# Optimization experiments

Measured on AMD Instinct MI355X. Metric: run time of the kernel, lower is better.

Reference implementation:

```python
import jax, jax.numpy as jnp
import numpy as np

# RReLU in eval mode acts as leaky-relu with slope (lower+upper)/2, defaults 1/8, 1/3
RRELU_SLOPE = (1.0 / 8.0 + 1.0 / 3.0) / 2.0

T, N, F, H, C, O, E = 8, 50000, 128, 128, 64, 2, 800000
HM1 = H - 1  # second GCN layer / MLP input width = hidden_feat - 1


def _glorot(k, shape):
    a = np.sqrt(6.0 / (shape[-2] + shape[-1])).astype(np.float32)
    return jax.random.uniform(k, shape, jnp.float32, -a, a)


def setup_inputs() -> dict:
    key = jax.random.key(0)
    ks = jax.random.split(key, 16)
    inp = {}
    inp["feats"] = jax.random.normal(ks[0], (T, N, F), jnp.float32)
    inp["src"] = jax.random.randint(ks[1], (E,), 0, N, jnp.int32)
    inp["dst"] = jax.random.randint(ks[2], (E,), 0, N, jnp.int32)
    # initial GCN weights (xavier_uniform as in reset_parameters)
    inp["W1_0"] = _glorot(ks[3], (F, H))
    inp["W2_0"] = _glorot(ks[4], (H, HM1))
    # mat-GRU cell 1 (rows=F, cols=H): gates stacked [z, r, h]
    inp["g1_W"] = jax.random.normal(ks[5], (3, F, F), jnp.float32) * 0.05
    inp["g1_U"] = jax.random.normal(ks[6], (3, F, F), jnp.float32) * 0.05
    inp["g1_b"] = jnp.zeros((3, F, H), jnp.float32)
    # mat-GRU cell 2 (rows=H, cols=H-1)
    inp["g2_W"] = jax.random.normal(ks[7], (3, H, H), jnp.float32) * 0.05
    inp["g2_U"] = jax.random.normal(ks[8], (3, H, H), jnp.float32) * 0.05
    inp["g2_b"] = jnp.zeros((3, H, HM1), jnp.float32)
    # MLP head
    inp["mlp_w1"] = _glorot(ks[9], (HM1, C))
    inp["mlp_b1"] = jnp.zeros((C,), jnp.float32)
    inp["mlp_w2"] = _glorot(ks[10], (C, O))
    inp["mlp_b2"] = jnp.zeros((O,), jnp.float32)
    return inp


def _mat_gru(gW, gU, gb, Wh):
    # EvolveGCN-O: weight matrix is both input and hidden of the GRU
    z = jax.nn.sigmoid(gW[0] @ Wh + gU[0] @ Wh + gb[0])
    r = jax.nn.sigmoid(gW[1] @ Wh + gU[1] @ Wh + gb[1])
    h_til = jnp.tanh(gW[2] @ Wh + gU[2] @ (r * Wh) + gb[2])
    return (1.0 - z) * Wh + z * h_til


def reference(feats, W1_0, W2_0, g1_W, g1_U, g1_b, g2_W, g2_U, g2_b,
              mlp_w1, mlp_b1, mlp_w2, mlp_b2, src, dst):
    n = feats.shape[1]
    ones = jnp.ones(src.shape, jnp.float32)
    deg_out = jax.ops.segment_sum(ones, src, num_segments=n)
    deg_in = jax.ops.segment_sum(ones, dst, num_segments=n)
    # symmetric GCN normalization D_out^-1/2 A D_in^-1/2 on edge list
    norm = (jax.lax.rsqrt(jnp.maximum(deg_out, 1.0))[src]
            * jax.lax.rsqrt(jnp.maximum(deg_in, 1.0))[dst])  # [E]

    def aggregate(x):  # x: [N, d] -> [N, d]
        return jax.ops.segment_sum(x[src] * norm[:, None], dst, num_segments=n)

    def step(carry, x):
        W1, W2, _ = carry
        W1 = _mat_gru(g1_W, g1_U, g1_b, W1)
        W2 = _mat_gru(g2_W, g2_U, g2_b, W2)
        h1 = aggregate(x @ W1)                      # [N, H]
        h1 = jnp.where(h1 >= 0, h1, RRELU_SLOPE * h1)  # RReLU (eval-mode)
        h2 = aggregate(h1 @ W2)                     # [N, H-1]
        return (W1, W2, h2), None

    feat0 = jnp.zeros((n, W2_0.shape[1]), feats.dtype)
    (W1, W2, feat_end), _ = jax.lax.scan(step, (W1_0, W2_0, feat0), feats)
    out = jnp.maximum(feat_end @ mlp_w1 + mlp_b1, 0.0) @ mlp_w2 + mlp_b2
    return out
```

## Files before the change

### kernel.cpp

```cpp
#include <hip/hip_runtime.h>


#define HM1 127

static constexpr float RRELU_SLOPE = (1.0f / 8.0f + 1.0f / 3.0f) * 0.5f;

__device__ __forceinline__ float sigmoidf_(float x) {
    return 1.0f / (1.0f + expf(-x));
}

__global__ __launch_bounds__(256) void prep_gates(
    const float* __restrict__ g1W, const float* __restrict__ g1U,
    const float* __restrict__ g2W, const float* __restrict__ g2U,
    float* __restrict__ AT)
{
    int t = blockIdx.x * 256 + threadIdx.x;
    int m = t >> 14;
    int k = (t >> 7) & 127;
    int i = t & 127;
    const float* W = (m < 4) ? g1W : g2W;
    const float* U = (m < 4) ? g1U : g2U;
    int which = m & 3;
    float v;
    if (which == 0)      v = W[i * 128 + k] + U[i * 128 + k];
    else if (which == 1) v = W[16384 + i * 128 + k] + U[16384 + i * 128 + k];
    else if (which == 2) v = W[32768 + i * 128 + k];
    else                 v = U[32768 + i * 128 + k];
    AT[t] = v;
}

__global__ __launch_bounds__(128) void gru_evolve(
    const float* __restrict__ W1_0, const float* __restrict__ W2_0,
    const float* __restrict__ AT,
    const float* __restrict__ g1b, const float* __restrict__ g2b,
    float* __restrict__ W1f, float* __restrict__ W2f)
{
    const int i = threadIdx.x;
    const int bid = blockIdx.x;
    const int cell = (bid >= 128) ? 1 : 0;
    const int c = cell ? (bid - 128) : bid;

    const float* A  = AT + cell * 4 * 16384;
    const float* A0 = A;
    const float* A1 = A + 16384;
    const float* B0 = A + 32768;
    const float* B1 = A + 49152;
    const float* gb = cell ? g2b : g1b;
    const int   ldb = cell ? HM1 : 128;
    const float* W0 = cell ? W2_0 : W1_0;
    const int   ldw = cell ? HM1 : 128;

    __shared__ float w[128];
    __shared__ float rw[128];

    const float zb = gb[i * ldb + c];
    const float rb = gb[128 * ldb + i * ldb + c];
    const float hb = gb[2 * 128 * ldb + i * ldb + c];
    float wi = W0[i * ldw + c];
    w[i] = wi;
    __syncthreads();

    for (int s = 0; s < 8; ++s) {
        float zacc = zb, racc = rb, tacc = hb;
        #pragma unroll 4
        for (int k = 0; k < 128; ++k) {
            float wk = w[k];
            zacc += A0[k * 128 + i] * wk;
            racc += A1[k * 128 + i] * wk;
            tacc += B0[k * 128 + i] * wk;
        }
        float r = sigmoidf_(racc);
        rw[i] = r * wi;
        __syncthreads();
        #pragma unroll 4
        for (int k = 0; k < 128; ++k)
            tacc += B1[k * 128 + i] * rw[k];
        float z = sigmoidf_(zacc);
        float t = tanhf(tacc);
        float nwi = (1.0f - z) * wi + z * t;
        __syncthreads();
        wi = nwi;
        w[i] = nwi;
        __syncthreads();
    }

    float* Wf = cell ? W2f : W1f;
    Wf[i * 128 + c] = wi;
}

__global__ __launch_bounds__(256) void small_matmul(
    const float* __restrict__ W2f, const float* __restrict__ mw1,
    float* __restrict__ W2m)
{
    int idx = blockIdx.x * 256 + threadIdx.x;
    int i = idx >> 6, j = idx & 63;
    float acc = 0.0f;
    for (int k = 0; k < HM1; ++k)
        acc += W2f[i * 128 + k] * mw1[k * 64 + j];
    W2m[idx] = acc;
}

__global__ __launch_bounds__(256) void deg_count(
    const int* __restrict__ src, const int* __restrict__ dst,
    int* __restrict__ degO, int* __restrict__ degI, int E)
{
    int e = blockIdx.x * 256 + threadIdx.x;
    if (e < E) {
        atomicAdd(&degO[src[e]], 1);
        atomicAdd(&degI[dst[e]], 1);
    }
}

__global__ __launch_bounds__(256) void rdeg_kernel(
    const int* __restrict__ degO, const int* __restrict__ degI,
    float* __restrict__ rdegO, float* __restrict__ rdegI, int N)
{
    int n = blockIdx.x * 256 + threadIdx.x;
    if (n < N) {
        rdegO[n] = rsqrtf(fmaxf((float)degO[n], 1.0f));
        rdegI[n] = rsqrtf(fmaxf((float)degI[n], 1.0f));
    }
}

__global__ __launch_bounds__(1024) void scan_kernel(
    const int* __restrict__ degI, int* __restrict__ row_ptr, int N)
{
    __shared__ int sums[1024];
    const int t = threadIdx.x;
    const int chunk = (N + 1023) / 1024;
    const int lo = t * chunk;
    const int hi = min(lo + chunk, N);
    int s = 0;
    for (int i = lo; i < hi; ++i) s += degI[i];
    sums[t] = s;
    __syncthreads();
    for (int off = 1; off < 1024; off <<= 1) {
        int v = (t >= off) ? sums[t - off] : 0;
        __syncthreads();
        sums[t] += v;
        __syncthreads();
    }
    int base = (t > 0) ? sums[t - 1] : 0;
    for (int i = lo; i < hi; ++i) {
        row_ptr[i] = base;
        base += degI[i];
    }
    if (t == 1023) row_ptr[N] = sums[1023];
}

__global__ __launch_bounds__(256) void build_csr(
    const int* __restrict__ src, const int* __restrict__ dst,
    const int* __restrict__ row_ptr, int* __restrict__ cursor,
    int* __restrict__ srcs, int E)
{
    int e = blockIdx.x * 256 + threadIdx.x;
    if (e < E) {
        int d = dst[e];
        int pos = row_ptr[d] + atomicAdd(&cursor[d], 1);
        srcs[pos] = src[e];
    }
}

__global__ __launch_bounds__(256) void gather128(
    const float* __restrict__ x, const int* __restrict__ srcs,
    const int* __restrict__ row_ptr, const float* __restrict__ rdegO,
    const float* __restrict__ rdegI, float* __restrict__ out, int N)
{
    int n = (blockIdx.x * 256 + threadIdx.x) >> 6;
    int lane = threadIdx.x & 63;
    if (n >= N) return;
    int lo = row_ptr[n], hi = row_ptr[n + 1];
    float ax = 0.0f, ay = 0.0f;
    for (int base = lo; base < hi; base += 64) {
        int cnt = min(hi - base, 64);
        int idx   = (lane < cnt) ? srcs[base + lane] : 0;
        float wgt = (lane < cnt) ? rdegO[idx] : 0.0f;
        int j = 0;
        for (; j + 4 <= cnt; j += 4) {
            int s0 = __shfl(idx, j + 0), s1 = __shfl(idx, j + 1);
            int s2 = __shfl(idx, j + 2), s3 = __shfl(idx, j + 3);
            float w0 = __shfl(wgt, j + 0), w1 = __shfl(wgt, j + 1);
            float w2 = __shfl(wgt, j + 2), w3 = __shfl(wgt, j + 3);
            float2 v0 = *reinterpret_cast<const float2*>(x + (size_t)s0 * 128 + lane * 2);
            float2 v1 = *reinterpret_cast<const float2*>(x + (size_t)s1 * 128 + lane * 2);
            float2 v2 = *reinterpret_cast<const float2*>(x + (size_t)s2 * 128 + lane * 2);
            float2 v3 = *reinterpret_cast<const float2*>(x + (size_t)s3 * 128 + lane * 2);
            ax += w0 * v0.x + w1 * v1.x + w2 * v2.x + w3 * v3.x;
            ay += w0 * v0.y + w1 * v1.y + w2 * v2.y + w3 * v3.y;
        }
        for (; j < cnt; ++j) {
            int s0 = __shfl(idx, j);
            float w0 = __shfl(wgt, j);
            float2 v0 = *reinterpret_cast<const float2*>(x + (size_t)s0 * 128 + lane * 2);
            ax += w0 * v0.x;
            ay += w0 * v0.y;
        }
    }
    float ri = rdegI[n];
    float2 o; o.x = ax * ri; o.y = ay * ri;
    *reinterpret_cast<float2*>(out + (size_t)n * 128 + lane * 2) = o;
}

__global__ __launch_bounds__(256) void gemm_rrelu(
    const float* __restrict__ X, const float* __restrict__ W,
    float* __restrict__ Y, int N)
{
    int row = blockIdx.x * 256 + threadIdx.x;
    int c0 = blockIdx.y * 64;
    if (row >= N) return;

    float acc[64];
    #pragma unroll
    for (int j = 0; j < 64; ++j) acc[j] = 0.0f;

    const float4* xr = reinterpret_cast<const float4*>(X + (size_t)row * 128);
    for (int k4 = 0; k4 < 32; ++k4) {
        float4 xv = xr[k4];
        const float* wr = W + (k4 * 4) * 128 + c0;
        #pragma unroll
        for (int j = 0; j < 64; ++j) acc[j] += xv.x * wr[j];
        wr += 128;
        #pragma unroll
        for (int j = 0; j < 64; ++j) acc[j] += xv.y * wr[j];
        wr += 128;
        #pragma unroll
        for (int j = 0; j < 64; ++j) acc[j] += xv.z * wr[j];
        wr += 128;
        #pragma unroll
        for (int j = 0; j < 64; ++j) acc[j] += xv.w * wr[j];
    }

    float* yr = Y + (size_t)row * 128 + c0;
    #pragma unroll
    for (int j = 0; j < 64; j += 4) {
        float4 v;
        v.x = acc[j + 0] >= 0.0f ? acc[j + 0] : RRELU_SLOPE * acc[j + 0];
        v.y = acc[j + 1] >= 0.0f ? acc[j + 1] : RRELU_SLOPE * acc[j + 1];
        v.z = acc[j + 2] >= 0.0f ? acc[j + 2] : RRELU_SLOPE * acc[j + 2];
        v.w = acc[j + 3] >= 0.0f ? acc[j + 3] : RRELU_SLOPE * acc[j + 3];
        *reinterpret_cast<float4*>(yr + j) = v;
    }
}

__global__ __launch_bounds__(256) void gemm_y(
    const float* __restrict__ H1, const float* __restrict__ W2m,
    const float* __restrict__ rdegO, float* __restrict__ Ys, int N)
{
    int row = blockIdx.x * 256 + threadIdx.x;
    if (row >= N) return;

    float acc[64];
    #pragma unroll
    for (int j = 0; j < 64; ++j) acc[j] = 0.0f;

    const float4* hr = reinterpret_cast<const float4*>(H1 + (size_t)row * 128);
    for (int k4 = 0; k4 < 32; ++k4) {
        float4 h = hr[k4];
        const float* wr = W2m + (k4 * 4) * 64;
        #pragma unroll
        for (int j = 0; j < 64; ++j) acc[j] += h.x * wr[j];
        wr += 64;
        #pragma unroll
        for (int j = 0; j < 64; ++j) acc[j] += h.y * wr[j];
        wr += 64;
        #pragma unroll
        for (int j = 0; j < 64; ++j) acc[j] += h.z * wr[j];
        wr += 64;
        #pragma unroll
        for (int j = 0; j < 64; ++j) acc[j] += h.w * wr[j];
    }

    float ro = rdegO[row];
    float* yr = Ys + (size_t)row * 64;
    #pragma unroll
    for (int j = 0; j < 64; j += 4) {
        float4 v;
        v.x = acc[j] * ro; v.y = acc[j + 1] * ro;
        v.z = acc[j + 2] * ro; v.w = acc[j + 3] * ro;
        *reinterpret_cast<float4*>(yr + j) = v;
    }
}

__global__ __launch_bounds__(256) void gather64_mlp(
    const float* __restrict__ Ys, const int* __restrict__ srcs,
    const int* __restrict__ row_ptr, const float* __restrict__ rdegI,
    const float* __restrict__ b1, const float* __restrict__ w2,
    const float* __restrict__ b2, float* __restrict__ out, int N)
{
    int n = (blockIdx.x * 256 + threadIdx.x) >> 6;
    int lane = threadIdx.x & 63;
    if (n >= N) return;
    int lo = row_ptr[n], hi = row_ptr[n + 1];
    float acc = 0.0f;
    for (int base = lo; base < hi; base += 64) {
        int cnt = min(hi - base, 64);
        int idx = (lane < cnt) ? srcs[base + lane] : 0;
        int j = 0;
        for (; j + 4 <= cnt; j += 4) {
            int s0 = __shfl(idx, j + 0), s1 = __shfl(idx, j + 1);
            int s2 = __shfl(idx, j + 2), s3 = __shfl(idx, j + 3);
            acc += Ys[(size_t)s0 * 64 + lane] + Ys[(size_t)s1 * 64 + lane]
                 + Ys[(size_t)s2 * 64 + lane] + Ys[(size_t)s3 * 64 + lane];
        }
        for (; j < cnt; ++j) {
            int s0 = __shfl(idx, j);
            acc += Ys[(size_t)s0 * 64 + lane];
        }
    }
    float z = acc * rdegI[n];
    float t = fmaxf(z + b1[lane], 0.0f);
    float p0 = t * w2[lane * 2 + 0];
    float p1 = t * w2[lane * 2 + 1];
    #pragma unroll
    for (int off = 32; off; off >>= 1) {
        p0 += __shfl_xor(p0, off);
        p1 += __shfl_xor(p1, off);
    }
    if (lane == 0) {
        out[(size_t)n * 2 + 0] = p0 + b2[0];
        out[(size_t)n * 2 + 1] = p1 + b2[1];
    }
}

extern "C" void kernel_launch(void* const* d_in, const int* in_sizes, int n_in,
                              void* d_out, int out_size, void* d_ws, size_t ws_size,
                              hipStream_t stream) {
    const float* feats = (const float*)d_in[0];
    const int*   src   = (const int*)d_in[1];
    const int*   dst   = (const int*)d_in[2];
    const float* W1_0  = (const float*)d_in[3];
    const float* W2_0  = (const float*)d_in[4];
    const float* g1W   = (const float*)d_in[5];
    const float* g1U   = (const float*)d_in[6];
    const float* g1b   = (const float*)d_in[7];
    const float* g2W   = (const float*)d_in[8];
    const float* g2U   = (const float*)d_in[9];
    const float* g2b   = (const float*)d_in[10];
    const float* mw1   = (const float*)d_in[11];
    const float* mb1   = (const float*)d_in[12];
    const float* mw2   = (const float*)d_in[13];
    const float* mb2   = (const float*)d_in[14];
    float* out = (float*)d_out;

    const int E = in_sizes[1];
    const int N = in_sizes[0] / (8 * 128);

    float* ws    = (float*)d_ws;
    float* W1f   = ws;
    float* W2f   = W1f + 16384;
    float* W2m   = W2f + 16384;
    float* AT    = W2m + 8192;
    float* rdegO = AT + 8 * 16384;
    float* rdegI = rdegO + N;
    int*   degO  = (int*)(rdegI + N);
    int*   degI  = degO + N;
    int*   cursor= degI + N;
    int*   row_ptr = cursor + N;
    int*   srcs  = row_ptr + N + 1;
    float* Sx    = (float*)(srcs + E);
    float* H1    = Sx + (size_t)N * 128;
    float* Ys    = Sx;

    hipMemsetAsync(degO, 0, sizeof(int) * 3 * (size_t)N, stream);
    deg_count<<<(E + 255) / 256, 256, 0, stream>>>(src, dst, degO, degI, E);
    rdeg_kernel<<<(N + 255) / 256, 256, 0, stream>>>(degO, degI, rdegO, rdegI, N);
    scan_kernel<<<1, 1024, 0, stream>>>(degI, row_ptr, N);
    build_csr<<<(E + 255) / 256, 256, 0, stream>>>(src, dst, row_ptr, cursor, srcs, E);

    prep_gates<<<512, 256, 0, stream>>>(g1W, g1U, g2W, g2U, AT);
    gru_evolve<<<255, 128, 0, stream>>>(W1_0, W2_0, AT, g1b, g2b, W1f, W2f);
    small_matmul<<<32, 256, 0, stream>>>(W2f, mw1, W2m);

    const float* x7 = feats + (size_t)7 * N * 128;
    int ngather = ((N * 64) + 255) / 256;
    gather128<<<ngather, 256, 0, stream>>>(x7, srcs, row_ptr, rdegO, rdegI, Sx, N);

    dim3 gg((N + 255) / 256, 2);
    gemm_rrelu<<<gg, 256, 0, stream>>>(Sx, W1f, H1, N);
    gemm_y<<<(N + 255) / 256, 256, 0, stream>>>(H1, W2m, rdegO, Ys, N);

    gather64_mlp<<<ngather, 256, 0, stream>>>(Ys, srcs, row_ptr, rdegI,
                                              mb1, mw2, mb2, out, N);
}
```

Measured before the change: 726.6 us.

## Merge independent setup kernels into phases and apply first GEMM before gathering

Independent setup kernels (degree counting, gate prep, GRU evolution, scan, rdeg, CSR build, small matmul) are combined into three multi-role launches so independent work runs concurrently and fewer launches are issued. The first layer is reordered to compute X@W1 scaled by rdegO before aggregation, so the gather only sums and then applies rdegI and RReLU, which removes per-edge weight shuffles. The gather loops are unrolled by 8 for more loads in flight. The trade-offs are that the scan now runs in a single 256-thread block alongside the GRU blocks, and that the GEMM now runs in the same launch as the CSR build.

```diff
diff --git a/kernel.cpp b/kernel.cpp
--- a/kernel.cpp
+++ b/kernel.cpp
@@ -9,162 +9,200 @@
     return 1.0f / (1.0f + expf(-x));
 }
 
-__global__ __launch_bounds__(256) void prep_gates(
+__global__ __launch_bounds__(256) void phase1(
+    const int* __restrict__ src, const int* __restrict__ dst,
+    int* __restrict__ degO, int* __restrict__ degI, int E, int nbE,
     const float* __restrict__ g1W, const float* __restrict__ g1U,
     const float* __restrict__ g2W, const float* __restrict__ g2U,
     float* __restrict__ AT)
 {
-    int t = blockIdx.x * 256 + threadIdx.x;
-    int m = t >> 14;
-    int k = (t >> 7) & 127;
-    int i = t & 127;
-    const float* W = (m < 4) ? g1W : g2W;
-    const float* U = (m < 4) ? g1U : g2U;
-    int which = m & 3;
-    float v;
-    if (which == 0)      v = W[i * 128 + k] + U[i * 128 + k];
-    else if (which == 1) v = W[16384 + i * 128 + k] + U[16384 + i * 128 + k];
-    else if (which == 2) v = W[32768 + i * 128 + k];
-    else                 v = U[32768 + i * 128 + k];
-    AT[t] = v;
-}
-
-__global__ __launch_bounds__(128) void gru_evolve(
+    int bid = blockIdx.x;
+    if (bid < nbE) {
+        int e = bid * 256 + threadIdx.x;
+        if (e < E) {
+            atomicAdd(&degO[src[e]], 1);
+            atomicAdd(&degI[dst[e]], 1);
+        }
+    } else {
+        int t = (bid - nbE) * 256 + threadIdx.x;
+        int m = t >> 14;
+        int k = (t >> 7) & 127;
+        int i = t & 127;
+        const float* W = (m < 4) ? g1W : g2W;
+        const float* U = (m < 4) ? g1U : g2U;
+        int which = m & 3;
+        float v;
+        if (which == 0)      v = W[i * 128 + k] + U[i * 128 + k];
+        else if (which == 1) v = W[16384 + i * 128 + k] + U[16384 + i * 128 + k];
+        else if (which == 2) v = W[32768 + i * 128 + k];
+        else                 v = U[32768 + i * 128 + k];
+        AT[t] = v;
+    }
+}
+
+__global__ __launch_bounds__(256) void phase2(
     const float* __restrict__ W1_0, const float* __restrict__ W2_0,
     const float* __restrict__ AT,
     const float* __restrict__ g1b, const float* __restrict__ g2b,
-    float* __restrict__ W1f, float* __restrict__ W2f)
-{
-    const int i = threadIdx.x;
-    const int bid = blockIdx.x;
-    const int cell = (bid >= 128) ? 1 : 0;
-    const int c = cell ? (bid - 128) : bid;
-
-    const float* A  = AT + cell * 4 * 16384;
-    const float* A0 = A;
-    const float* A1 = A + 16384;
-    const float* B0 = A + 32768;
-    const float* B1 = A + 49152;
-    const float* gb = cell ? g2b : g1b;
-    const int   ldb = cell ? HM1 : 128;
-    const float* W0 = cell ? W2_0 : W1_0;
-    const int   ldw = cell ? HM1 : 128;
-
-    __shared__ float w[128];
-    __shared__ float rw[128];
-
-    const float zb = gb[i * ldb + c];
-    const float rb = gb[128 * ldb + i * ldb + c];
-    const float hb = gb[2 * 128 * ldb + i * ldb + c];
-    float wi = W0[i * ldw + c];
-    w[i] = wi;
-    __syncthreads();
-
-    for (int s = 0; s < 8; ++s) {
-        float zacc = zb, racc = rb, tacc = hb;
-        #pragma unroll 4
-        for (int k = 0; k < 128; ++k) {
-            float wk = w[k];
-            zacc += A0[k * 128 + i] * wk;
-            racc += A1[k * 128 + i] * wk;
-            tacc += B0[k * 128 + i] * wk;
-        }
-        float r = sigmoidf_(racc);
-        rw[i] = r * wi;
+    float* __restrict__ W1f, float* __restrict__ W2f,
+    const int* __restrict__ degO, const int* __restrict__ degI,
+    float* __restrict__ rdegO, float* __restrict__ rdegI,
+    int* __restrict__ row_ptr, int N)
+{
+    __shared__ float smem[512];
+    int bid = blockIdx.x;
+    if (bid < 128) {
+        const int half = threadIdx.x >> 7;
+        const int i = threadIdx.x & 127;
+        int c = bid * 2 + half;
+        if (c > 254) c = 254;
+        const int cell = (c >= 128) ? 1 : 0;
+        const int cc = cell ? (c - 128) : c;
+
+        const float* A  = AT + cell * 4 * 16384;
+        const float* A0 = A;
+        const float* A1 = A + 16384;
+        const float* B0 = A + 32768;
+        const float* B1 = A + 49152;
+        const float* gb = cell ? g2b : g1b;
+        const int   ldb = cell ? HM1 : 128;
+        const float* W0 = cell ? W2_0 : W1_0;
+        const int   ldw = cell ? HM1 : 128;
+
+        float* w  = smem + half * 128;
+        float* rw = smem + 256 + half * 128;
+
+        const float zb = gb[i * ldb + cc];
+        const float rb = gb[128 * ldb + i * ldb + cc];
+        const float hb = gb[2 * 128 * ldb + i * ldb + cc];
+        float wi = W0[i * ldw + cc];
+        w[i] = wi;
         __syncthreads();
-        #pragma unroll 4
-        for (int k = 0; k < 128; ++k)
-            tacc += B1[k * 128 + i] * rw[k];
-        float z = sigmoidf_(zacc);
-        float t = tanhf(tacc);
-        float nwi = (1.0f - z) * wi + z * t;
+
+        for (int s = 0; s < 8; ++s) {
+            float zacc = zb, racc = rb, tacc = hb;
+            #pragma unroll 4
+            for (int k = 0; k < 128; ++k) {
+                float wk = w[k];
+                zacc += A0[k * 128 + i] * wk;
+                racc += A1[k * 128 + i] * wk;
+                tacc += B0[k * 128 + i] * wk;
+            }
+            float r = sigmoidf_(racc);
+            rw[i] = r * wi;
+            __syncthreads();
+            #pragma unroll 4
+            for (int k = 0; k < 128; ++k)
+                tacc += B1[k * 128 + i] * rw[k];
+            float z = sigmoidf_(zacc);
+            float t = tanhf(tacc);
+            float nwi = (1.0f - z) * wi + z * t;
+            __syncthreads();
+            wi = nwi;
+            w[i] = nwi;
+            __syncthreads();
+        }
+        float* Wf = cell ? W2f : W1f;
+        Wf[i * 128 + cc] = wi;
+    } else if (bid == 128) {
+        int* sums = (int*)smem;
+        const int t = threadIdx.x;
+        const int chunk = (N + 255) / 256;
+        const int lo = t * chunk;
+        const int hi = min(lo + chunk, N);
+        int s = 0;
+        for (int i2 = lo; i2 < hi; ++i2) s += degI[i2];
+        sums[t] = s;
         __syncthreads();
-        wi = nwi;
-        w[i] = nwi;
-        __syncthreads();
-    }
-
-    float* Wf = cell ? W2f : W1f;
-    Wf[i * 128 + c] = wi;
-}
-
-__global__ __launch_bounds__(256) void small_matmul(
+        for (int off = 1; off < 256; off <<= 1) {
+            int v = (t >= off) ? sums[t - off] : 0;
+            __syncthreads();
+            sums[t] += v;
+            __syncthreads();
+        }
+        int base = (t > 0) ? sums[t - 1] : 0;
+        for (int i2 = lo; i2 < hi; ++i2) {
+            row_ptr[i2] = base;
+            base += degI[i2];
+        }
+        if (t == 255) row_ptr[N] = sums[255];
+    } else {
+        int n = (bid - 129) * 256 + threadIdx.x;
+        if (n < N) {
+            rdegO[n] = rsqrtf(fmaxf((float)degO[n], 1.0f));
+            rdegI[n] = rsqrtf(fmaxf((float)degI[n], 1.0f));
+        }
+    }
+}
+
+__global__ __launch_bounds__(256) void phase3(
+    const int* __restrict__ src, const int* __restrict__ dst,
+    const int* __restrict__ row_ptr, int* __restrict__ cursor,
+    int* __restrict__ srcs, int E, int nbE,
+    const float* __restrict__ x7, const float* __restrict__ W1f,
+    const float* __restrict__ rdegO, float* __restrict__ Zs, int N, int nbN,
     const float* __restrict__ W2f, const float* __restrict__ mw1,
     float* __restrict__ W2m)
 {
-    int idx = blockIdx.x * 256 + threadIdx.x;
-    int i = idx >> 6, j = idx & 63;
-    float acc = 0.0f;
-    for (int k = 0; k < HM1; ++k)
-        acc += W2f[i * 128 + k] * mw1[k * 64 + j];
-    W2m[idx] = acc;
-}
-
-__global__ __launch_bounds__(256) void deg_count(
-    const int* __restrict__ src, const int* __restrict__ dst,
-    int* __restrict__ degO, int* __restrict__ degI, int E)
-{
-    int e = blockIdx.x * 256 + threadIdx.x;
-    if (e < E) {
-        atomicAdd(&degO[src[e]], 1);
-        atomicAdd(&degI[dst[e]], 1);
-    }
-}
-
-__global__ __launch_bounds__(256) void rdeg_kernel(
-    const int* __restrict__ degO, const int* __restrict__ degI,
-    float* __restrict__ rdegO, float* __restrict__ rdegI, int N)
-{
-    int n = blockIdx.x * 256 + threadIdx.x;
-    if (n < N) {
-        rdegO[n] = rsqrtf(fmaxf((float)degO[n], 1.0f));
-        rdegI[n] = rsqrtf(fmaxf((float)degI[n], 1.0f));
-    }
-}
-
-__global__ __launch_bounds__(1024) void scan_kernel(
-    const int* __restrict__ degI, int* __restrict__ row_ptr, int N)
-{
-    __shared__ int sums[1024];
-    const int t = threadIdx.x;
-    const int chunk = (N + 1023) / 1024;
-    const int lo = t * chunk;
-    const int hi = min(lo + chunk, N);
-    int s = 0;
-    for (int i = lo; i < hi; ++i) s += degI[i];
-    sums[t] = s;
-    __syncthreads();
-    for (int off = 1; off < 1024; off <<= 1) {
-        int v = (t >= off) ? sums[t - off] : 0;
-        __syncthreads();
-        sums[t] += v;
-        __syncthreads();
-    }
-    int base = (t > 0) ? sums[t - 1] : 0;
-    for (int i = lo; i < hi; ++i) {
-        row_ptr[i] = base;
-        base += degI[i];
-    }
-    if (t == 1023) row_ptr[N] = sums[1023];
-}
-
-__global__ __launch_bounds__(256) void build_csr(
-    const int* __restrict__ src, const int* __restrict__ dst,
-    const int* __restrict__ row_ptr, int* __restrict__ cursor,
-    int* __restrict__ srcs, int E)
-{
-    int e = blockIdx.x * 256 + threadIdx.x;
-    if (e < E) {
-        int d = dst[e];
-        int pos = row_ptr[d] + atomicAdd(&cursor[d], 1);
-        srcs[pos] = src[e];
+    int bid = blockIdx.x;
+    if (bid < nbE) {
+        int e = bid * 256 + threadIdx.x;
+        if (e < E) {
+            int d = dst[e];
+            int pos = row_ptr[d] + atomicAdd(&cursor[d], 1);
+            srcs[pos] = src[e];
+        }
+    } else if (bid < nbE + 2 * nbN) {
+        int b = bid - nbE;
+        int half = b & 1;
+        int row = (b >> 1) * 256 + threadIdx.x;
+        int c0 = half * 64;
+        if (row >= N) return;
+
+        float acc[64];
+        #pragma unroll
+        for (int j = 0; j < 64; ++j) acc[j] = 0.0f;
+
+        const float4* xr = reinterpret_cast<const float4*>(x7 + (size_t)row * 128);
+        for (int k4 = 0; k4 < 32; ++k4) {
+            float4 xv = xr[k4];
+            const float* wr = W1f + (k4 * 4) * 128 + c0;
+            #pragma unroll
+            for (int j = 0; j < 64; ++j) acc[j] += xv.x * wr[j];
+            wr += 128;
+            #pragma unroll
+            for (int j = 0; j < 64; ++j) acc[j] += xv.y * wr[j];
+            wr += 128;
+            #pragma unroll
+            for (int j = 0; j < 64; ++j) acc[j] += xv.z * wr[j];
+            wr += 128;
+            #pragma unroll
+            for (int j = 0; j < 64; ++j) acc[j] += xv.w * wr[j];
+        }
+
+        float ro = rdegO[row];
+        float* zr = Zs + (size_t)row * 128 + c0;
+        #pragma unroll
+        for (int j = 0; j < 64; j += 4) {
+            float4 v;
+            v.x = acc[j] * ro; v.y = acc[j + 1] * ro;
+            v.z = acc[j + 2] * ro; v.w = acc[j + 3] * ro;
+            *reinterpret_cast<float4*>(zr + j) = v;
+        }
+    } else {
+        int idx = (bid - nbE - 2 * nbN) * 256 + threadIdx.x;
+        int i = idx >> 6, j = idx & 63;
+        float acc = 0.0f;
+        for (int k = 0; k < HM1; ++k)
+            acc += W2f[i * 128 + k] * mw1[k * 64 + j];
+        W2m[idx] = acc;
     }
 }
 
 __global__ __launch_bounds__(256) void gather128(
-    const float* __restrict__ x, const int* __restrict__ srcs,
-    const int* __restrict__ row_ptr, const float* __restrict__ rdegO,
-    const float* __restrict__ rdegI, float* __restrict__ out, int N)
+    const float* __restrict__ Zs, const int* __restrict__ srcs,
+    const int* __restrict__ row_ptr, const float* __restrict__ rdegI,
+    float* __restrict__ H1, int N)
 {
     int n = (blockIdx.x * 256 + threadIdx.x) >> 6;
     int lane = threadIdx.x & 63;
@@ -173,73 +211,37 @@
     float ax = 0.0f, ay = 0.0f;
     for (int base = lo; base < hi; base += 64) {
         int cnt = min(hi - base, 64);
-        int idx   = (lane < cnt) ? srcs[base + lane] : 0;
-        float wgt = (lane < cnt) ? rdegO[idx] : 0.0f;
+        int idx = (lane < cnt) ? srcs[base + lane] : 0;
         int j = 0;
-        for (; j + 4 <= cnt; j += 4) {
+        for (; j + 8 <= cnt; j += 8) {
             int s0 = __shfl(idx, j + 0), s1 = __shfl(idx, j + 1);
             int s2 = __shfl(idx, j + 2), s3 = __shfl(idx, j + 3);
-            float w0 = __shfl(wgt, j + 0), w1 = __shfl(wgt, j + 1);
-            float w2 = __shfl(wgt, j + 2), w3 = __shfl(wgt, j + 3);
-            float2 v0 = *reinterpret_cast<const float2*>(x + (size_t)s0 * 128 + lane * 2);
-            float2 v1 = *reinterpret_cast<const float2*>(x + (size_t)s1 * 128 + lane * 2);
-            float2 v2 = *reinterpret_cast<const float2*>(x + (size_t)s2 * 128 + lane * 2);
-            float2 v3 = *reinterpret_cast<const float2*>(x + (size_t)s3 * 128 + lane * 2);
-            ax += w0 * v0.x + w1 * v1.x + w2 * v2.x + w3 * v3.x;
-            ay += w0 * v0.y + w1 * v1.y + w2 * v2.y + w3 * v3.y;
+            int s4 = __shfl(idx, j + 4), s5 = __shfl(idx, j + 5);
+            int s6 = __shfl(idx, j + 6), s7 = __shfl(idx, j + 7);
+            float2 v0 = *reinterpret_cast<const float2*>(Zs + (size_t)s0 * 128 + lane * 2);
+            float2 v1 = *reinterpret_cast<const float2*>(Zs + (size_t)s1 * 128 + lane * 2);
+            float2 v2 = *reinterpret_cast<const float2*>(Zs + (size_t)s2 * 128 + lane * 2);
+            float2 v3 = *reinterpret_cast<const float2*>(Zs + (size_t)s3 * 128 + lane * 2);
+            float2 v4 = *reinterpret_cast<const float2*>(Zs + (size_t)s4 * 128 + lane * 2);
+            float2 v5 = *reinterpret_cast<const float2*>(Zs + (size_t)s5 * 128 + lane * 2);
+            float2 v6 = *reinterpret_cast<const float2*>(Zs + (size_t)s6 * 128 + lane * 2);
+            float2 v7 = *reinterpret_cast<const float2*>(Zs + (size_t)s7 * 128 + lane * 2);
+            ax += v0.x + v1.x + v2.x + v3.x + v4.x + v5.x + v6.x + v7.x;
+            ay += v0.y + v1.y + v2.y + v3.y + v4.y + v5.y + v6.y + v7.y;
         }
         for (; j < cnt; ++j) {
             int s0 = __shfl(idx, j);
-            float w0 = __shfl(wgt, j);
-            float2 v0 = *reinterpret_cast<const float2*>(x + (size_t)s0 * 128 + lane * 2);
-            ax += w0 * v0.x;
-            ay += w0 * v0.y;
+            float2 v0 = *reinterpret_cast<const float2*>(Zs + (size_t)s0 * 128 + lane * 2);
+            ax += v0.x;
+            ay += v0.y;
         }
     }
     float ri = rdegI[n];
-    float2 o; o.x = ax * ri; o.y = ay * ri;
-    *reinterpret_cast<float2*>(out + (size_t)n * 128 + lane * 2) = o;
-}
-
-__global__ __launch_bounds__(256) void gemm_rrelu(
-    const float* __restrict__ X, const float* __restrict__ W,
-    float* __restrict__ Y, int N)
-{
-    int row = blockIdx.x * 256 + threadIdx.x;
-    int c0 = blockIdx.y * 64;
-    if (row >= N) return;
-
-    float acc[64];
-    #pragma unroll
-    for (int j = 0; j < 64; ++j) acc[j] = 0.0f;
-
-    const float4* xr = reinterpret_cast<const float4*>(X + (size_t)row * 128);
-    for (int k4 = 0; k4 < 32; ++k4) {
-        float4 xv = xr[k4];
-        const float* wr = W + (k4 * 4) * 128 + c0;
-        #pragma unroll
-        for (int j = 0; j < 64; ++j) acc[j] += xv.x * wr[j];
-        wr += 128;
-        #pragma unroll
-        for (int j = 0; j < 64; ++j) acc[j] += xv.y * wr[j];
-        wr += 128;
-        #pragma unroll
-        for (int j = 0; j < 64; ++j) acc[j] += xv.z * wr[j];
-        wr += 128;
-        #pragma unroll
-        for (int j = 0; j < 64; ++j) acc[j] += xv.w * wr[j];
-    }
-
-    float* yr = Y + (size_t)row * 128 + c0;
-    #pragma unroll
-    for (int j = 0; j < 64; j += 4) {
-        float4 v;
-        v.x = acc[j + 0] >= 0.0f ? acc[j + 0] : RRELU_SLOPE * acc[j + 0];
-        v.y = acc[j + 1] >= 0.0f ? acc[j + 1] : RRELU_SLOPE * acc[j + 1];
-        v.z = acc[j + 2] >= 0.0f ? acc[j + 2] : RRELU_SLOPE * acc[j + 2];
-        v.w = acc[j + 3] >= 0.0f ? acc[j + 3] : RRELU_SLOPE * acc[j + 3];
-        *reinterpret_cast<float4*>(yr + j) = v;
-    }
+    ax *= ri; ay *= ri;
+    ax = ax >= 0.0f ? ax : RRELU_SLOPE * ax;
+    ay = ay >= 0.0f ? ay : RRELU_SLOPE * ay;
+    float2 o; o.x = ax; o.y = ay;
+    *reinterpret_cast<float2*>(H1 + (size_t)n * 128 + lane * 2) = o;
 }
 
 __global__ __launch_bounds__(256) void gemm_y(
@@ -296,11 +298,15 @@
         int cnt = min(hi - base, 64);
         int idx = (lane < cnt) ? srcs[base + lane] : 0;
         int j = 0;
-        for (; j + 4 <= cnt; j += 4) {
+        for (; j + 8 <= cnt; j += 8) {
             int s0 = __shfl(idx, j + 0), s1 = __shfl(idx, j + 1);
             int s2 = __shfl(idx, j + 2), s3 = __shfl(idx, j + 3);
+            int s4 = __shfl(idx, j + 4), s5 = __shfl(idx, j + 5);
+            int s6 = __shfl(idx, j + 6), s7 = __shfl(idx, j + 7);
             acc += Ys[(size_t)s0 * 64 + lane] + Ys[(size_t)s1 * 64 + lane]
-                 + Ys[(size_t)s2 * 64 + lane] + Ys[(size_t)s3 * 64 + lane];
+                 + Ys[(size_t)s2 * 64 + lane] + Ys[(size_t)s3 * 64 + lane]
+                 + Ys[(size_t)s4 * 64 + lane] + Ys[(size_t)s5 * 64 + lane]
+                 + Ys[(size_t)s6 * 64 + lane] + Ys[(size_t)s7 * 64 + lane];
         }
         for (; j < cnt; ++j) {
             int s0 = __shfl(idx, j);
@@ -344,6 +350,8 @@
 
     const int E = in_sizes[1];
     const int N = in_sizes[0] / (8 * 128);
+    const int nbE = (E + 255) / 256;
+    const int nbN = (N + 255) / 256;
 
     float* ws    = (float*)d_ws;
     float* W1f   = ws;
@@ -357,27 +365,28 @@
     int*   cursor= degI + N;
     int*   row_ptr = cursor + N;
     int*   srcs  = row_ptr + N + 1;
-    float* Sx    = (float*)(srcs + E);
-    float* H1    = Sx + (size_t)N * 128;
-    float* Ys    = Sx;
+    float* Zs    = (float*)(srcs + E);
+    float* H1    = Zs + (size_t)N * 128;
+    float* Ys    = Zs;
+
+    const float* x7 = feats + (size_t)7 * N * 128;
 
     hipMemsetAsync(degO, 0, sizeof(int) * 3 * (size_t)N, stream);
-    deg_count<<<(E + 255) / 256, 256, 0, stream>>>(src, dst, degO, degI, E);
-    rdeg_kernel<<<(N + 255) / 256, 256, 0, stream>>>(degO, degI, rdegO, rdegI, N);
-    scan_kernel<<<1, 1024, 0, stream>>>(degI, row_ptr, N);
-    build_csr<<<(E + 255) / 256, 256, 0, stream>>>(src, dst, row_ptr, cursor, srcs, E);
-
-    prep_gates<<<512, 256, 0, stream>>>(g1W, g1U, g2W, g2U, AT);
-    gru_evolve<<<255, 128, 0, stream>>>(W1_0, W2_0, AT, g1b, g2b, W1f, W2f);
-    small_matmul<<<32, 256, 0, stream>>>(W2f, mw1, W2m);
-
-    const float* x7 = feats + (size_t)7 * N * 128;
+
+    phase1<<<nbE + 512, 256, 0, stream>>>(src, dst, degO, degI, E, nbE,
+                                          g1W, g1U, g2W, g2U, AT);
+
+    phase2<<<129 + nbN, 256, 0, stream>>>(W1_0, W2_0, AT, g1b, g2b, W1f, W2f,
+                                          degO, degI, rdegO, rdegI, row_ptr, N);
+
+    phase3<<<nbE + 2 * nbN + 32, 256, 0, stream>>>(
+        src, dst, row_ptr, cursor, srcs, E, nbE,
+        x7, W1f, rdegO, Zs, N, nbN, W2f, mw1, W2m);
+
     int ngather = ((N * 64) + 255) / 256;
-    gather128<<<ngather, 256, 0, stream>>>(x7, srcs, row_ptr, rdegO, rdegI, Sx, N);
-
-    dim3 gg((N + 255) / 256, 2);
-    gemm_rrelu<<<gg, 256, 0, stream>>>(Sx, W1f, H1, N);
-    gemm_y<<<(N + 255) / 256, 256, 0, stream>>>(H1, W2m, rdegO, Ys, N);
+    gather128<<<ngather, 256, 0, stream>>>(Zs, srcs, row_ptr, rdegI, H1, N);
+
+    gemm_y<<<nbN, 256, 0, stream>>>(H1, W2m, rdegO, Ys, N);
 
     gather64_mlp<<<ngather, 256, 0, stream>>>(Ys, srcs, row_ptr, rdegI,
                                               mb1, mw2, mb2, out, N);
```

New measurement: 635.7 us. 1.14x faster.
